# Optimization experiments

Hardware: AMD Instinct MI355X
Metric: run time of the kernel (lower is better)

Reference implementation:

```python
import jax, jax.numpy as jnp
import numpy as np

D_MODEL = 1024
N_HEADS = 16
D_K = D_MODEL // N_HEADS


def setup_inputs() -> dict:
    key = jax.random.key(0)
    ks = jax.random.split(key, 11)
    B, S = 2, 2048
    scale = 0.02
    inp = {
        "q": jax.random.normal(ks[0], (B, S, D_MODEL), jnp.float32),
        "k": jax.random.normal(ks[1], (B, S, D_MODEL), jnp.float32),
        "v": jax.random.normal(ks[2], (B, S, D_MODEL), jnp.float32),
        "w_q": jax.random.normal(ks[3], (D_MODEL, D_MODEL), jnp.float32) * scale,
        "b_q": jnp.zeros((D_MODEL,), jnp.float32),
        "w_k": jax.random.normal(ks[4], (D_MODEL, D_MODEL), jnp.float32) * scale,
        "b_k": jnp.zeros((D_MODEL,), jnp.float32),
        "w_v": jax.random.normal(ks[5], (D_MODEL, D_MODEL), jnp.float32) * scale,
        "b_v": jnp.zeros((D_MODEL,), jnp.float32),
        "w_o": jax.random.normal(ks[6], (D_MODEL, D_MODEL), jnp.float32) * scale,
        "b_o": jnp.zeros((D_MODEL,), jnp.float32),
    }
    return inp


def reference(q, k, v, w_q, b_q, w_k, b_k, w_v, b_v, w_o, b_o):
    B, S, _ = q.shape
    # projections (torch Linear: x @ W.T + b); split into heads -> [B, H, S, d]
    def proj(x, w, b):
        return (x @ w.T + b).reshape(B, S, N_HEADS, D_K).transpose(0, 2, 1, 3)
    qh = proj(q, w_q, b_q)
    kh = proj(k, w_k, b_k)
    vh = proj(v, w_v, b_v)
    scores = jnp.einsum("bhqd,bhkd->bhqk", qh, kh) / jnp.sqrt(
        jnp.asarray(D_K, jnp.float32))
    attn = jax.nn.softmax(scores, axis=-1)  # dropout = identity (eval)
    out = jnp.einsum("bhqk,bhkd->bhqd", attn, vh)
    out = out.transpose(0, 2, 1, 3).reshape(B, S, D_MODEL)
    return out @ w_o.T + b_o
```

## Files before the change

### kernel.cpp

```cpp
#include <hip/hip_runtime.h>

typedef unsigned short u16;
typedef unsigned int u32;
typedef __attribute__((ext_vector_type(4))) unsigned short u16x4;
typedef __attribute__((ext_vector_type(8))) unsigned short u16x8;
typedef __attribute__((ext_vector_type(8))) __bf16 bf16x8;
typedef __attribute__((ext_vector_type(4))) float f32x4;
typedef __attribute__((ext_vector_type(16))) float f32x16;

#define SEQ 2048
#define DMODEL 1024
#define LDP 3072
#define MM (DMODEL * DMODEL)
#define SC 0.18033688f

__device__ __forceinline__ u16 f2bf(float f) {
  unsigned u = __builtin_bit_cast(unsigned, f);
  u = (u + 0x7fffu + ((u >> 16) & 1u)) >> 16;
  return (u16)u;
}

__device__ __forceinline__ u32 cvtpk(float lo, float hi) {
  u32 r;
  asm volatile("v_cvt_pk_bf16_f32 %0, %1, %2" : "=v"(r) : "v"(lo), "v"(hi));
  return r;
}

__device__ __forceinline__ float fexp2(float x) {
#if __has_builtin(__builtin_amdgcn_exp2f)
  return __builtin_amdgcn_exp2f(x);
#else
  return exp2f(x);
#endif
}

__device__ __forceinline__ bf16x8 ldbf8(const u16* p) {
  return __builtin_bit_cast(bf16x8, *(const u16x8*)p);
}
__device__ __forceinline__ bf16x8 ldbf8c(const char* p) {
  return __builtin_bit_cast(bf16x8, *(const u16x8*)p);
}

__device__ __forceinline__ f32x4 mfma16(bf16x8 a, bf16x8 b, f32x4 c) {
  return __builtin_amdgcn_mfma_f32_16x16x32_bf16(a, b, c, 0, 0, 0);
}
__device__ __forceinline__ f32x16 mfma32(bf16x8 a, bf16x8 b, f32x16 c) {
  return __builtin_amdgcn_mfma_f32_32x32x16_bf16(a, b, c, 0, 0, 0);
}

__device__ __forceinline__ void gl16(const void* g, void* l) {
  __builtin_amdgcn_global_load_lds(
      (__attribute__((address_space(1))) void*)(size_t)g,
      (__attribute__((address_space(3))) void*)l, 16, 0, 0);
}

__global__ void cast_all_k(const float* __restrict__ q, const float* __restrict__ k,
                           const float* __restrict__ v, const float* __restrict__ wq,
                           const float* __restrict__ wk, const float* __restrict__ wv,
                           const float* __restrict__ wo, u16* __restrict__ dq,
                           u16* __restrict__ dk, u16* __restrict__ dv,
                           u16* __restrict__ wqkv, u16* __restrict__ wob) {
  int b = blockIdx.x;
  const float* s;
  u16* d;
  if (b < 6144) {
    const int z = b >> 11;
    s = z == 0 ? q : z == 1 ? k : v;
    d = z == 0 ? dq : z == 1 ? dk : dv;
    b &= 2047;
  } else {
    const int z = (b - 6144) >> 9;
    s = z == 0 ? wq : z == 1 ? wk : z == 2 ? wv : wo;
    d = z < 3 ? wqkv + (size_t)z * MM : wob;
    b = (b - 6144) & 511;
  }
  const size_t i = ((size_t)b * blockDim.x + threadIdx.x) * 8;
  const float4 a = *(const float4*)(s + i);
  const float4 c = *(const float4*)(s + i + 4);
  u16x8 o;
  o[0] = f2bf(a.x); o[1] = f2bf(a.y); o[2] = f2bf(a.z); o[3] = f2bf(a.w);
  o[4] = f2bf(c.x); o[5] = f2bf(c.y); o[6] = f2bf(c.z); o[7] = f2bf(c.w);
  *(u16x8*)(d + i) = o;
}

template <int OMODE>
__device__ __forceinline__ void gemm_bt_body(const u16* __restrict__ A,
                                             const u16* __restrict__ Bw,
                                             const float* __restrict__ bias,
                                             void* __restrict__ Cv, const int K,
                                             const int ldc, const int ncol0,
                                             const int m0, const int n0,
                                             const float osc) {
  __shared__ u16 As[128 * 32];
  __shared__ u16 Bs[128 * 32];
  const int tid = threadIdx.x;
  const int lane = tid & 63;
  const int w = tid >> 6;
  const int l15 = lane & 15;
  const int lg = lane >> 4;

  f32x4 acc[4][4] = {};

  const int arow = (w >> 1) * 64 + l15;
  const int brow = (w & 1) * 64 + l15;
  const int kfb = lg * 16;

  const int strow = w * 32 + (lane >> 2);
  const u16* Ag = A + (size_t)(m0 + strow) * K + (lane & 3) * 8;
  const u16* Bg = Bw + (size_t)(n0 + strow) * K + (lane & 3) * 8;
  const size_t rstep = (size_t)16 * K;
  char* AsL0 = (char*)As + w * 32 * 64;
  char* AsL1 = AsL0 + 16 * 64;
  char* BsL0 = (char*)Bs + w * 32 * 64;
  char* BsL1 = BsL0 + 16 * 64;

  for (int k0 = 0; k0 < K; k0 += 32) {
    __syncthreads();
    gl16(Ag + k0, AsL0);
    gl16(Ag + k0 + rstep, AsL1);
    gl16(Bg + k0, BsL0);
    gl16(Bg + k0 + rstep, BsL1);
    __syncthreads();
    bf16x8 af[4], bfv[4];
#pragma unroll
    for (int t = 0; t < 4; ++t) {
      af[t] = ldbf8c((char*)As + (arow + t * 16) * 64 + kfb);
      bfv[t] = ldbf8c((char*)Bs + (brow + t * 16) * 64 + kfb);
    }
    __builtin_amdgcn_s_setprio(1);
#pragma unroll
    for (int i = 0; i < 4; ++i)
#pragma unroll
      for (int j = 0; j < 4; ++j) acc[i][j] = mfma16(af[i], bfv[j], acc[i][j]);
    __builtin_amdgcn_s_setprio(0);
  }

  const int mrow = (w >> 1) * 64 + lg * 4;
  const int ncol = (w & 1) * 64 + l15;
#pragma unroll
  for (int j = 0; j < 4; ++j) {
    const int gn = n0 + ncol + j * 16;
    const float bia = bias[gn];
#pragma unroll
    for (int i = 0; i < 4; ++i) {
      const int gmb = m0 + mrow + i * 16;
#pragma unroll
      for (int r = 0; r < 4; ++r) {
        const float val = (acc[i][j][r] + bia) * osc;
        const int gm = gmb + r;
        if (OMODE == 0) {
          ((float*)Cv)[(size_t)gm * ldc + gn] = val;
        } else if (OMODE == 1) {
          ((u16*)Cv)[(size_t)gm * ldc + ncol0 + gn] = f2bf(val);
        } else {
          const int bb = gm >> 11, ss = gm & 2047;
          const int hh = gn >> 6, dd = gn & 63;
          ((u16*)Cv)[(((size_t)(bb * 16 + hh) * 64 + dd) << 11) + ss] = f2bf(val);
        }
      }
    }
  }
}

__global__ __launch_bounds__(256, 3) void gemm_qkv_k(
    const u16* __restrict__ qb, const u16* __restrict__ kb,
    const u16* __restrict__ vb, const u16* __restrict__ wqkv,
    const float* __restrict__ bq, const float* __restrict__ bk,
    const float* __restrict__ bv, u16* __restrict__ proj, u16* __restrict__ vtb) {
  const int b = blockIdx.x;
  const int xcd = b & 7;
  const int i = b >> 3;
  const int z = i >> 5;
  const int j = i & 31;
  const int m0 = (xcd * 4 + (j >> 3)) * 128;
  const int n0 = (j & 7) * 128;
  if (z == 2)
    gemm_bt_body<2>(vb, wqkv + 2 * (size_t)MM, bv, vtb, DMODEL, 0, 0, m0, n0,
                    1.0f);
  else
    gemm_bt_body<1>(z == 0 ? qb : kb, wqkv + (size_t)z * MM, z == 0 ? bq : bk,
                    proj, DMODEL, LDP, z * DMODEL, m0, n0, z == 0 ? SC : 1.0f);
}

__global__ __launch_bounds__(256, 3) void gemm_o_k(const u16* __restrict__ attnb,
                                                   const u16* __restrict__ wob,
                                                   const float* __restrict__ bo,
                                                   float* __restrict__ out) {
  const int b = blockIdx.x;
  const int xcd = b & 7;
  const int i = b >> 3;
  const int m0 = (xcd * 4 + (i >> 3)) * 128;
  const int n0 = (i & 7) * 128;
  gemm_bt_body<0>(attnb, wob, bo, out, DMODEL, DMODEL, 0, m0, n0, 1.0f);
}

__global__ __launch_bounds__(512, 2) void attn_k(const u16* __restrict__ proj,
                                                 const u16* __restrict__ vtb,
                                                 u16* __restrict__ outa) {
  __shared__ __align__(16) char smem[65536];
  const int b = blockIdx.x;
  const int slot = b >> 3;
  const int bh = (b & 7) * 4 + (slot >> 4);
  const int qB = (slot & 15) * 128;
  const int tid = threadIdx.x;
  const int lane = tid & 63;
  const int w = tid >> 6;
  const int g = w >> 2;
  const int wg = w & 3;
  const int tg = tid & 255;
  const size_t rb = (size_t)(bh >> 4) * SEQ;
  const int h = bh & 15;
  const int l31 = lane & 31;
  const int hi = lane >> 5;
  const int swzk = (l31 & 7) << 4;
  const int swzv = (l31 & 15) << 3;

  char* const ksb = smem + g * 32768;
  char* const vsb = ksb + 16384;

  const u16* qp = proj + (rb + qB + wg * 32 + l31) * LDP + h * 64 + hi * 8;
  bf16x8 qf[4];
#pragma unroll
  for (int km = 0; km < 4; ++km) qf[km] = ldbf8(qp + km * 16);

  const int srow = tg >> 2;
  const int scol = (tg & 3) * 32;
  const int scel = scol >> 1;
  const int kz0 = srow * 128 + (scol ^ ((srow & 7) << 4));
  const int kz1 = srow * 128 + ((scol + 16) ^ ((srow & 7) << 4));
  const int vz0 = srow * 128 + (scol ^ ((srow & 15) << 3));
  const int vz1 = srow * 128 + ((scol + 8) ^ ((srow & 15) << 3));
  const int vz2 = srow * 128 + ((scol + 16) ^ ((srow & 15) << 3));
  const int vz3 = srow * 128 + ((scol + 24) ^ ((srow & 15) << 3));
  const u16* kg = proj + rb * LDP + DMODEL + h * 64;
  const u16* vg = vtb + (size_t)bh * 64 * SEQ;
  const int kvbase = g * (SEQ / 2);

  u16x8 ka0, ka1, va0, va1;
  {
    const u16* kr = kg + (size_t)(kvbase + srow) * LDP + scel;
    ka0 = *(const u16x8*)kr;
    ka1 = *(const u16x8*)(kr + 8);
    const u16* vr = vg + (size_t)srow * SEQ + kvbase + scel;
    va0 = *(const u16x8*)vr;
    va1 = *(const u16x8*)(vr + 8);
  }

  f32x16 oa0 = {}, oa1 = {};
  float lrun = 0.f;
  int p = 0;

  for (int it = 0; it < SEQ / 128; ++it) {
    {
      char* kd = ksb + p * 8192;
      char* vd = vsb + p * 8192;
      *(u16x8*)(kd + kz0) = ka0;
      *(u16x8*)(kd + kz1) = ka1;
      *(u16x4*)(vd + vz0) = *(u16x4*)&va0;
      *(u16x4*)(vd + vz1) = *((u16x4*)&va0 + 1);
      *(u16x4*)(vd + vz2) = *(u16x4*)&va1;
      *(u16x4*)(vd + vz3) = *((u16x4*)&va1 + 1);
    }
    __syncthreads();
    if (it + 1 < SEQ / 128) {
      const int kvn = kvbase + (it + 1) * 64;
      const u16* kr = kg + (size_t)(kvn + srow) * LDP + scel;
      ka0 = *(const u16x8*)kr;
      ka1 = *(const u16x8*)(kr + 8);
      const u16* vr = vg + (size_t)srow * SEQ + kvn + scel;
      va0 = *(const u16x8*)vr;
      va1 = *(const u16x8*)(vr + 8);
    }
    const char* kp = ksb + p * 8192;
    const char* vp = vsb + p * 8192;
    f32x16 s0 = {}, s1 = {};
    __builtin_amdgcn_s_setprio(1);
#pragma unroll
    for (int km = 0; km < 4; ++km) {
      const int co = (km * 32 + hi * 16) ^ swzk;
      const bf16x8 k0 = ldbf8c(kp + l31 * 128 + co);
      const bf16x8 k1 = ldbf8c(kp + (32 + l31) * 128 + co);
      s0 = mfma32(k0, qf[km], s0);
      s1 = mfma32(k1, qf[km], s1);
    }
    __builtin_amdgcn_s_setprio(0);

#pragma unroll
    for (int r = 0; r < 16; ++r) s0[r] = fexp2(s0[r]);
#pragma unroll
    for (int r = 0; r < 16; ++r) s1[r] = fexp2(s1[r]);
    float rs = (((s0[0] + s0[1]) + (s0[2] + s0[3])) +
                ((s0[4] + s0[5]) + (s0[6] + s0[7]))) +
               (((s0[8] + s0[9]) + (s0[10] + s0[11])) +
                ((s0[12] + s0[13]) + (s0[14] + s0[15])));
    rs += (((s1[0] + s1[1]) + (s1[2] + s1[3])) +
           ((s1[4] + s1[5]) + (s1[6] + s1[7]))) +
          (((s1[8] + s1[9]) + (s1[10] + s1[11])) +
           ((s1[12] + s1[13]) + (s1[14] + s1[15])));
    rs += __shfl_xor(rs, 32);
    lrun += rs;

    __builtin_amdgcn_s_setprio(1);
#define PCHUNK(SV, G, CB)                                                \
    {                                                                    \
      u16x8 pbu;                                                         \
      ((u32*)&pbu)[0] = cvtpk(SV[G + 0], SV[G + 1]);                     \
      ((u32*)&pbu)[1] = cvtpk(SV[G + 2], SV[G + 3]);                     \
      ((u32*)&pbu)[2] = cvtpk(SV[G + 4], SV[G + 5]);                     \
      ((u32*)&pbu)[3] = cvtpk(SV[G + 6], SV[G + 7]);                     \
      const bf16x8 pb = __builtin_bit_cast(bf16x8, pbu);                 \
      const int vc0 = ((CB) + 8 * hi) ^ swzv;                            \
      const int vc1 = ((CB) + 16 + 8 * hi) ^ swzv;                       \
      const char* vr0 = vp + l31 * 128;                                  \
      const char* vr1 = vp + (32 + l31) * 128;                           \
      u16x8 vf0, vf1;                                                    \
      *(u16x4*)&vf0       = *(const u16x4*)(vr0 + vc0);                  \
      *((u16x4*)&vf0 + 1) = *(const u16x4*)(vr0 + vc1);                  \
      *(u16x4*)&vf1       = *(const u16x4*)(vr1 + vc0);                  \
      *((u16x4*)&vf1 + 1) = *(const u16x4*)(vr1 + vc1);                  \
      oa0 = mfma32(__builtin_bit_cast(bf16x8, vf0), pb, oa0);            \
      oa1 = mfma32(__builtin_bit_cast(bf16x8, vf1), pb, oa1);            \
    }
    PCHUNK(s0, 0, 0)
    PCHUNK(s0, 8, 32)
    PCHUNK(s1, 0, 64)
    PCHUNK(s1, 8, 96)
#undef PCHUNK
    __builtin_amdgcn_s_setprio(0);
    p ^= 1;
  }

  float* sc = (float*)smem;
  __syncthreads();
  if (g == 1) {
    const int col = wg * 64 + lane;
#pragma unroll
    for (int r = 0; r < 16; ++r) sc[r * 256 + col] = oa0[r];
#pragma unroll
    for (int r = 0; r < 16; ++r) sc[(16 + r) * 256 + col] = oa1[r];
    sc[32 * 256 + col] = lrun;
  }
  __syncthreads();
  if (g == 0) {
    const int col = wg * 64 + lane;
#pragma unroll
    for (int r = 0; r < 16; ++r) oa0[r] += sc[r * 256 + col];
#pragma unroll
    for (int r = 0; r < 16; ++r) oa1[r] += sc[(16 + r) * 256 + col];
    lrun += sc[32 * 256 + col];

    const float invl = 1.0f / lrun;
    u16* orow = outa + (rb + qB + wg * 32 + l31) * DMODEL + h * 64 + hi * 4;
#pragma unroll
    for (int gg = 0; gg < 4; ++gg) {
      u16x4 st0, st1;
      ((u32*)&st0)[0] = cvtpk(oa0[4 * gg + 0] * invl, oa0[4 * gg + 1] * invl);
      ((u32*)&st0)[1] = cvtpk(oa0[4 * gg + 2] * invl, oa0[4 * gg + 3] * invl);
      *(u16x4*)(orow + 8 * gg) = st0;
      ((u32*)&st1)[0] = cvtpk(oa1[4 * gg + 0] * invl, oa1[4 * gg + 1] * invl);
      ((u32*)&st1)[1] = cvtpk(oa1[4 * gg + 2] * invl, oa1[4 * gg + 3] * invl);
      *(u16x4*)(orow + 32 + 8 * gg) = st1;
    }
  }
}

extern "C" void kernel_launch(void* const* d_in, const int* in_sizes, int n_in,
                              void* d_out, int out_size, void* d_ws, size_t ws_size,
                              hipStream_t stream) {
  const float* q  = (const float*)d_in[0];
  const float* k  = (const float*)d_in[1];
  const float* v  = (const float*)d_in[2];
  const float* wq = (const float*)d_in[3];
  const float* bq = (const float*)d_in[4];
  const float* wk = (const float*)d_in[5];
  const float* bk = (const float*)d_in[6];
  const float* wv = (const float*)d_in[7];
  const float* bv = (const float*)d_in[8];
  const float* wo = (const float*)d_in[9];
  const float* bo = (const float*)d_in[10];

  const size_t NTOK = (size_t)2 * SEQ;
  const size_t NELE = NTOK * DMODEL;
  u16* qb    = (u16*)d_ws;
  u16* kb    = qb + NELE;
  u16* vb    = kb + NELE;
  u16* wqkv  = vb + NELE;
  u16* wob   = wqkv + 3 * (size_t)MM;
  u16* projb = wob + (size_t)MM;
  u16* vtb   = projb + NTOK * LDP;
  u16* attnb = qb;

  cast_all_k<<<8192, 256, 0, stream>>>(q, k, v, wq, wk, wv, wo, qb, kb, vb,
                                       wqkv, wob);
  gemm_qkv_k<<<768, 256, 0, stream>>>(qb, kb, vb, wqkv, bq, bk, bv, projb, vtb);
  attn_k<<<512, 512, 0, stream>>>(projb, vtb, attnb);
  gemm_o_k<<<256, 256, 0, stream>>>(attnb, wob, bo, (float*)d_out);
}
```

Before: 127.8 us.

## Process 64 query rows per wave in attention to double K/V tile reuse

The attention kernel now has each wave handle two 32-row query sub-tiles (256 queries per block instead of 128), reusing every K and V fragment read from LDS for two MFMAs. The grid shrinks from 512 to 256 blocks, and the cross-group reduction runs in two passes. This halves LDS and global K/V traffic per query. In exchange it doubles accumulator registers, which may lower occupancy, and leaves only 256 blocks, which may underfill the GPU's compute units.

New measurement: 118.1 us. 1.08x faster.

```diff
diff --git a/kernel.cpp b/kernel.cpp
--- a/kernel.cpp
+++ b/kernel.cpp
@@ -200,8 +200,8 @@
   __shared__ __align__(16) char smem[65536];
   const int b = blockIdx.x;
   const int slot = b >> 3;
-  const int bh = (b & 7) * 4 + (slot >> 4);
-  const int qB = (slot & 15) * 128;
+  const int bh = (b & 7) * 4 + (slot >> 3);
+  const int qB = (slot & 7) * 256;
   const int tid = threadIdx.x;
   const int lane = tid & 63;
   const int w = tid >> 6;
@@ -218,10 +218,15 @@
   char* const ksb = smem + g * 32768;
   char* const vsb = ksb + 16384;
 
-  const u16* qp = proj + (rb + qB + wg * 32 + l31) * LDP + h * 64 + hi * 8;
-  bf16x8 qf[4];
-#pragma unroll
-  for (int km = 0; km < 4; ++km) qf[km] = ldbf8(qp + km * 16);
+  const int qW = qB + wg * 64;
+  const u16* qpA = proj + (rb + qW + l31) * LDP + h * 64 + hi * 8;
+  const u16* qpB = qpA + (size_t)32 * LDP;
+  bf16x8 qfA[4], qfB[4];
+#pragma unroll
+  for (int km = 0; km < 4; ++km) {
+    qfA[km] = ldbf8(qpA + km * 16);
+    qfB[km] = ldbf8(qpB + km * 16);
+  }
 
   const int srow = tg >> 2;
   const int scol = (tg & 3) * 32;
@@ -246,8 +251,8 @@
     va1 = *(const u16x8*)(vr + 8);
   }
 
-  f32x16 oa0 = {}, oa1 = {};
-  float lrun = 0.f;
+  f32x16 oaA0 = {}, oaA1 = {}, oaB0 = {}, oaB1 = {};
+  float lrunA = 0.f, lrunB = 0.f;
   int p = 0;
 
   for (int it = 0; it < SEQ / 128; ++it) {
@@ -273,42 +278,53 @@
     }
     const char* kp = ksb + p * 8192;
     const char* vp = vsb + p * 8192;
-    f32x16 s0 = {}, s1 = {};
+    f32x16 sA0 = {}, sA1 = {}, sB0 = {}, sB1 = {};
     __builtin_amdgcn_s_setprio(1);
 #pragma unroll
     for (int km = 0; km < 4; ++km) {
       const int co = (km * 32 + hi * 16) ^ swzk;
       const bf16x8 k0 = ldbf8c(kp + l31 * 128 + co);
       const bf16x8 k1 = ldbf8c(kp + (32 + l31) * 128 + co);
-      s0 = mfma32(k0, qf[km], s0);
-      s1 = mfma32(k1, qf[km], s1);
+      sA0 = mfma32(k0, qfA[km], sA0);
+      sB0 = mfma32(k0, qfB[km], sB0);
+      sA1 = mfma32(k1, qfA[km], sA1);
+      sB1 = mfma32(k1, qfB[km], sB1);
     }
     __builtin_amdgcn_s_setprio(0);
 
 #pragma unroll
-    for (int r = 0; r < 16; ++r) s0[r] = fexp2(s0[r]);
-#pragma unroll
-    for (int r = 0; r < 16; ++r) s1[r] = fexp2(s1[r]);
-    float rs = (((s0[0] + s0[1]) + (s0[2] + s0[3])) +
-                ((s0[4] + s0[5]) + (s0[6] + s0[7]))) +
-               (((s0[8] + s0[9]) + (s0[10] + s0[11])) +
-                ((s0[12] + s0[13]) + (s0[14] + s0[15])));
-    rs += (((s1[0] + s1[1]) + (s1[2] + s1[3])) +
-           ((s1[4] + s1[5]) + (s1[6] + s1[7]))) +
-          (((s1[8] + s1[9]) + (s1[10] + s1[11])) +
-           ((s1[12] + s1[13]) + (s1[14] + s1[15])));
-    rs += __shfl_xor(rs, 32);
-    lrun += rs;
+    for (int r = 0; r < 16; ++r) sA0[r] = fexp2(sA0[r]);
+#pragma unroll
+    for (int r = 0; r < 16; ++r) sA1[r] = fexp2(sA1[r]);
+#pragma unroll
+    for (int r = 0; r < 16; ++r) sB0[r] = fexp2(sB0[r]);
+#pragma unroll
+    for (int r = 0; r < 16; ++r) sB1[r] = fexp2(sB1[r]);
+#define SUM16(V)                                                        \
+    ((((V[0] + V[1]) + (V[2] + V[3])) + ((V[4] + V[5]) + (V[6] + V[7]))) + \
+     (((V[8] + V[9]) + (V[10] + V[11])) + ((V[12] + V[13]) + (V[14] + V[15]))))
+    float rsA = SUM16(sA0) + SUM16(sA1);
+    float rsB = SUM16(sB0) + SUM16(sB1);
+#undef SUM16
+    rsA += __shfl_xor(rsA, 32);
+    rsB += __shfl_xor(rsB, 32);
+    lrunA += rsA;
+    lrunB += rsB;
 
     __builtin_amdgcn_s_setprio(1);
-#define PCHUNK(SV, G, CB)                                                \
+#define PCHUNK2(SA, SB, G, CB)                                           \
     {                                                                    \
-      u16x8 pbu;                                                         \
-      ((u32*)&pbu)[0] = cvtpk(SV[G + 0], SV[G + 1]);                     \
-      ((u32*)&pbu)[1] = cvtpk(SV[G + 2], SV[G + 3]);                     \
-      ((u32*)&pbu)[2] = cvtpk(SV[G + 4], SV[G + 5]);                     \
-      ((u32*)&pbu)[3] = cvtpk(SV[G + 6], SV[G + 7]);                     \
-      const bf16x8 pb = __builtin_bit_cast(bf16x8, pbu);                 \
+      u16x8 pbuA, pbuB;                                                  \
+      ((u32*)&pbuA)[0] = cvtpk(SA[G + 0], SA[G + 1]);                    \
+      ((u32*)&pbuA)[1] = cvtpk(SA[G + 2], SA[G + 3]);                    \
+      ((u32*)&pbuA)[2] = cvtpk(SA[G + 4], SA[G + 5]);                    \
+      ((u32*)&pbuA)[3] = cvtpk(SA[G + 6], SA[G + 7]);                    \
+      ((u32*)&pbuB)[0] = cvtpk(SB[G + 0], SB[G + 1]);                    \
+      ((u32*)&pbuB)[1] = cvtpk(SB[G + 2], SB[G + 3]);                    \
+      ((u32*)&pbuB)[2] = cvtpk(SB[G + 4], SB[G + 5]);                    \
+      ((u32*)&pbuB)[3] = cvtpk(SB[G + 6], SB[G + 7]);                    \
+      const bf16x8 pbA = __builtin_bit_cast(bf16x8, pbuA);               \
+      const bf16x8 pbB = __builtin_bit_cast(bf16x8, pbuB);               \
       const int vc0 = ((CB) + 8 * hi) ^ swzv;                            \
       const int vc1 = ((CB) + 16 + 8 * hi) ^ swzv;                       \
       const char* vr0 = vp + l31 * 128;                                  \
@@ -318,48 +334,79 @@
       *((u16x4*)&vf0 + 1) = *(const u16x4*)(vr0 + vc1);                  \
       *(u16x4*)&vf1       = *(const u16x4*)(vr1 + vc0);                  \
       *((u16x4*)&vf1 + 1) = *(const u16x4*)(vr1 + vc1);                  \
-      oa0 = mfma32(__builtin_bit_cast(bf16x8, vf0), pb, oa0);            \
-      oa1 = mfma32(__builtin_bit_cast(bf16x8, vf1), pb, oa1);            \
-    }
-    PCHUNK(s0, 0, 0)
-    PCHUNK(s0, 8, 32)
-    PCHUNK(s1, 0, 64)
-    PCHUNK(s1, 8, 96)
-#undef PCHUNK
+      const bf16x8 v0 = __builtin_bit_cast(bf16x8, vf0);                 \
+      const bf16x8 v1 = __builtin_bit_cast(bf16x8, vf1);                 \
+      oaA0 = mfma32(v0, pbA, oaA0);                                      \
+      oaB0 = mfma32(v0, pbB, oaB0);                                      \
+      oaA1 = mfma32(v1, pbA, oaA1);                                      \
+      oaB1 = mfma32(v1, pbB, oaB1);                                      \
+    }
+    PCHUNK2(sA0, sB0, 0, 0)
+    PCHUNK2(sA0, sB0, 8, 32)
+    PCHUNK2(sA1, sB1, 0, 64)
+    PCHUNK2(sA1, sB1, 8, 96)
+#undef PCHUNK2
     __builtin_amdgcn_s_setprio(0);
     p ^= 1;
   }
 
   float* sc = (float*)smem;
+  const int col = wg * 64 + lane;
   __syncthreads();
   if (g == 1) {
-    const int col = wg * 64 + lane;
-#pragma unroll
-    for (int r = 0; r < 16; ++r) sc[r * 256 + col] = oa0[r];
-#pragma unroll
-    for (int r = 0; r < 16; ++r) sc[(16 + r) * 256 + col] = oa1[r];
-    sc[32 * 256 + col] = lrun;
+#pragma unroll
+    for (int r = 0; r < 16; ++r) sc[r * 256 + col] = oaA0[r];
+#pragma unroll
+    for (int r = 0; r < 16; ++r) sc[(16 + r) * 256 + col] = oaA1[r];
+    sc[32 * 256 + col] = lrunA;
   }
   __syncthreads();
   if (g == 0) {
-    const int col = wg * 64 + lane;
-#pragma unroll
-    for (int r = 0; r < 16; ++r) oa0[r] += sc[r * 256 + col];
-#pragma unroll
-    for (int r = 0; r < 16; ++r) oa1[r] += sc[(16 + r) * 256 + col];
-    lrun += sc[32 * 256 + col];
-
-    const float invl = 1.0f / lrun;
-    u16* orow = outa + (rb + qB + wg * 32 + l31) * DMODEL + h * 64 + hi * 4;
+#pragma unroll
+    for (int r = 0; r < 16; ++r) oaA0[r] += sc[r * 256 + col];
+#pragma unroll
+    for (int r = 0; r < 16; ++r) oaA1[r] += sc[(16 + r) * 256 + col];
+    lrunA += sc[32 * 256 + col];
+  }
+  __syncthreads();
+  if (g == 1) {
+#pragma unroll
+    for (int r = 0; r < 16; ++r) sc[r * 256 + col] = oaB0[r];
+#pragma unroll
+    for (int r = 0; r < 16; ++r) sc[(16 + r) * 256 + col] = oaB1[r];
+    sc[32 * 256 + col] = lrunB;
+  }
+  __syncthreads();
+  if (g == 0) {
+#pragma unroll
+    for (int r = 0; r < 16; ++r) oaB0[r] += sc[r * 256 + col];
+#pragma unroll
+    for (int r = 0; r < 16; ++r) oaB1[r] += sc[(16 + r) * 256 + col];
+    lrunB += sc[32 * 256 + col];
+
+    const float invA = 1.0f / lrunA;
+    u16* orowA = outa + (rb + qW + l31) * DMODEL + h * 64 + hi * 4;
 #pragma unroll
     for (int gg = 0; gg < 4; ++gg) {
       u16x4 st0, st1;
-      ((u32*)&st0)[0] = cvtpk(oa0[4 * gg + 0] * invl, oa0[4 * gg + 1] * invl);
-      ((u32*)&st0)[1] = cvtpk(oa0[4 * gg + 2] * invl, oa0[4 * gg + 3] * invl);
-      *(u16x4*)(orow + 8 * gg) = st0;
-      ((u32*)&st1)[0] = cvtpk(oa1[4 * gg + 0] * invl, oa1[4 * gg + 1] * invl);
-      ((u32*)&st1)[1] = cvtpk(oa1[4 * gg + 2] * invl, oa1[4 * gg + 3] * invl);
-      *(u16x4*)(orow + 32 + 8 * gg) = st1;
+      ((u32*)&st0)[0] = cvtpk(oaA0[4 * gg + 0] * invA, oaA0[4 * gg + 1] * invA);
+      ((u32*)&st0)[1] = cvtpk(oaA0[4 * gg + 2] * invA, oaA0[4 * gg + 3] * invA);
+      *(u16x4*)(orowA + 8 * gg) = st0;
+      ((u32*)&st1)[0] = cvtpk(oaA1[4 * gg + 0] * invA, oaA1[4 * gg + 1] * invA);
+      ((u32*)&st1)[1] = cvtpk(oaA1[4 * gg + 2] * invA, oaA1[4 * gg + 3] * invA);
+      *(u16x4*)(orowA + 32 + 8 * gg) = st1;
+    }
+    const float invB = 1.0f / lrunB;
+    u16* orowB = orowA + (size_t)32 * DMODEL;
+#pragma unroll
+    for (int gg = 0; gg < 4; ++gg) {
+      u16x4 st0, st1;
+      ((u32*)&st0)[0] = cvtpk(oaB0[4 * gg + 0] * invB, oaB0[4 * gg + 1] * invB);
+      ((u32*)&st0)[1] = cvtpk(oaB0[4 * gg + 2] * invB, oaB0[4 * gg + 3] * invB);
+      *(u16x4*)(orowB + 8 * gg) = st0;
+      ((u32*)&st1)[0] = cvtpk(oaB1[4 * gg + 0] * invB, oaB1[4 * gg + 1] * invB);
+      ((u32*)&st1)[1] = cvtpk(oaB1[4 * gg + 2] * invB, oaB1[4 * gg + 3] * invB);
+      *(u16x4*)(orowB + 32 + 8 * gg) = st1;
     }
   }
 }
@@ -393,6 +440,6 @@
   cast_all_k<<<8192, 256, 0, stream>>>(q, k, v, wq, wk, wv, wo, qb, kb, vb,
                                        wqkv, wob);
   gemm_qkv_k<<<768, 256, 0, stream>>>(qb, kb, vb, wqkv, bq, bk, bv, projb, vtb);
-  attn_k<<<512, 512, 0, stream>>>(projb, vtb, attnb);
+  attn_k<<<256, 512, 0, stream>>>(projb, vtb, attnb);
   gemm_o_k<<<256, 256, 0, stream>>>(attnb, wob, bo, (float*)d_out);
 }
```
